# Kernel optimization log

Hardware: AMD Instinct MI355X
Metric: run time of the kernel (lower is better)

The kernel has to match this reference:

```python
import jax, jax.numpy as jnp
import numpy as np


def setup_inputs() -> dict:
    key = jax.random.key(0)
    ks = jax.random.split(key, 6)
    B, S, H, F, E = 4, 2048, 1024, 4096, 8
    x = jax.random.normal(ks[0], (B, S, H), dtype=jnp.float32)
    Wr = jax.random.normal(ks[1], (H, E), dtype=jnp.float32) * (1.0 / np.sqrt(H))
    br = jnp.zeros((E,), dtype=jnp.float32)
    W1 = jax.random.normal(ks[2], (E, H, F), dtype=jnp.float32) * (1.0 / np.sqrt(H))
    b1 = jnp.zeros((E, F), dtype=jnp.float32)
    W2 = jax.random.normal(ks[3], (E, F, H), dtype=jnp.float32) * (1.0 / np.sqrt(F))
    b2 = jnp.zeros((E, H), dtype=jnp.float32)
    b_buf = jnp.zeros((E,), dtype=jnp.float32)  # load-balancing bias buffer, zero-init
    return {"x": x, "b_buf": b_buf, "Wr": Wr, "br": br,
            "W1": W1, "b1": b1, "W2": W2, "b2": b2, "k": 2}


def reference(x, b_buf, Wr, br, W1, b1, W2, b2, k):
    # Router
    scores = jnp.einsum('bsh,he->bse', x, Wr) + br          # [B,S,E]
    probs = jax.nn.softmax(scores, axis=-1)
    # load_balancing: expert selection uses biased scores (b_buf pre-update)
    _, expert_id = jax.lax.top_k(probs + b_buf, k)          # [B,S,k] int
    # combine weights use unbiased probs
    p, _ = jax.lax.top_k(probs, k)                          # [B,S,k]
    # Dense-dispatch reference: run every expert MLP on all tokens,
    # then select via one-hot mask (same math as gather/scatter dispatch).
    h1 = jnp.einsum('bsh,ehf->ebsf', x, W1) + b1[:, None, None, :]
    h1 = jax.nn.gelu(h1, approximate=False)                 # torch nn.GELU = exact
    out_e = jnp.einsum('ebsf,efh->ebsh', h1, W2) + b2[:, None, None, :]
    E = W1.shape[0]
    onehot = (expert_id[None, :, :, :] == jnp.arange(E)[:, None, None, None]).astype(x.dtype)  # [E,B,S,k]
    out_k = jnp.einsum('ebsk,ebsh->bskh', onehot, out_e)    # scatter-combine per slot
    w = p / jnp.sum(p, axis=-1, keepdims=True)              # normalize top-k probs
    return jnp.einsum('bsk,bskh->bsh', w, out_k)
```

## Files before the change

kernel.cpp:

```cpp
#include <hip/hip_runtime.h>
#include <stdint.h>

#define NTOK 8192
#define H_ 1024
#define F_ 4096
#define E_ 8
#define VCAP 18432
#define VMBLK 72
#define MT 144
#define NCOMP 16384

using f32x4  = __attribute__((ext_vector_type(4))) float;
using short8 = __attribute__((ext_vector_type(8))) short;

typedef __attribute__((address_space(1))) const uint32_t gu32;
typedef __attribute__((address_space(3))) uint32_t lu32;

__device__ __forceinline__ void glds16(const void* g, void* l) {
  __builtin_amdgcn_global_load_lds((gu32*)g, (lu32*)l, 16, 0, 0);
}

__device__ __forceinline__ ushort f2bf(float f) {
  union { float f; uint32_t u; } v; v.f = f;
  uint32_t r = (v.u + 0x7FFFu + ((v.u >> 16) & 1u)) >> 16;
  return (ushort)r;
}

__device__ __forceinline__ float gelu_t(float x) {
  float u = 0.7978845608028654f * (x + 0.044715f * x * x * x);
  float e = exp2f(u * 2.885390081777927f);
  float th = 1.0f - 2.0f / (1.0f + e);
  return 0.5f * x * (1.0f + th);
}

__global__ __launch_bounds__(256) void k_prep(const float* __restrict__ W1,
                                              const float* __restrict__ W2,
                                              ushort* __restrict__ W1T,
                                              ushort* __restrict__ W2T,
                                              const float* __restrict__ x,
                                              const float* __restrict__ Wr,
                                              const float* __restrict__ br,
                                              const float* __restrict__ bbuf,
                                              int* cnt, int* te, float* tw,
                                              int* cur, int* tok, float* wl,
                                              int* v2c) {
  int bid = blockIdx.x;
  if (bid < VMBLK) {
    int i = bid * 256 + threadIdx.x;
    if (i < E_) { cnt[i] = 0; cur[i] = 0; }
    if (i < VCAP) { tok[i] = -1; wl[i] = 0.f; v2c[i] = -1; }
  }
  if (bid >= 16384) {
    int wid = threadIdx.x >> 6, lane = threadIdx.x & 63;
    int t = (bid - 16384) * 4 + wid;
    const float* xp = x + (size_t)t * H_;
    double acc[E_];
#pragma unroll
    for (int e = 0; e < E_; e++) acc[e] = 0.0;
    for (int j = lane; j < H_; j += 64) {
      float xv = xp[j];
      const float4 w0 = *(const float4*)&Wr[j * 8];
      const float4 w1 = *(const float4*)&Wr[j * 8 + 4];
      acc[0] += (double)xv * (double)w0.x;
      acc[1] += (double)xv * (double)w0.y;
      acc[2] += (double)xv * (double)w0.z;
      acc[3] += (double)xv * (double)w0.w;
      acc[4] += (double)xv * (double)w1.x;
      acc[5] += (double)xv * (double)w1.y;
      acc[6] += (double)xv * (double)w1.z;
      acc[7] += (double)xv * (double)w1.w;
    }
#pragma unroll
    for (int e = 0; e < E_; e++)
      for (int s = 32; s > 0; s >>= 1) acc[e] += __shfl_xor(acc[e], s);
    if (lane == 0) {
      double s[E_], m = -1e300;
      for (int e = 0; e < E_; e++) { s[e] = acc[e] + (double)br[e]; if (s[e] > m) m = s[e]; }
      double pe[E_], sum = 0.0;
      for (int e = 0; e < E_; e++) { pe[e] = exp(s[e] - m); sum += pe[e]; }
      double pr[E_], bb[E_];
      for (int e = 0; e < E_; e++) { pr[e] = pe[e] / sum; bb[e] = pr[e] + (double)bbuf[e]; }
      int e0 = 0;
      for (int e = 1; e < E_; e++) if (bb[e] > bb[e0]) e0 = e;
      int e1 = (e0 == 0) ? 1 : 0;
      for (int e = 0; e < E_; e++) if (e != e0 && bb[e] > bb[e1]) e1 = e;
      int a0 = 0;
      for (int e = 1; e < E_; e++) if (pr[e] > pr[a0]) a0 = e;
      int a1 = (a0 == 0) ? 1 : 0;
      for (int e = 0; e < E_; e++) if (e != a0 && pr[e] > pr[a1]) a1 = e;
      double iv = 1.0 / (pr[a0] + pr[a1]);
      te[t * 2] = e0; te[t * 2 + 1] = e1;
      tw[t * 2] = (float)(pr[a0] * iv); tw[t * 2 + 1] = (float)(pr[a1] * iv);
      atomicAdd(&cnt[e0], 1); atomicAdd(&cnt[e1], 1);
    }
    return;
  }
  const float* W; ushort* WT; int R, C, nx, t;
  if (bid < 8192) { W = W1; WT = W1T; R = 1024; C = 4096; nx = 64; t = bid; }
  else            { W = W2; WT = W2T; R = 4096; C = 1024; nx = 16; t = bid - 8192; }
  int e = t >> 10, r = t & 1023;
  int c0 = (r % nx) * 64, r0 = (r / nx) * 64;

  __shared__ float tb[64][65];
  const float* Wp = W + (size_t)e * R * C;
  ushort* Tp = WT + (size_t)e * R * C;
  int tx = threadIdx.x & 15, ty = threadIdx.x >> 4;
#pragma unroll
  for (int i = 0; i < 4; i++) {
    int lr = ty + i * 16;
    const float4 v = *(const float4*)&Wp[(size_t)(r0 + lr) * C + c0 + tx * 4];
    tb[lr][tx * 4 + 0] = v.x; tb[lr][tx * 4 + 1] = v.y;
    tb[lr][tx * 4 + 2] = v.z; tb[lr][tx * 4 + 3] = v.w;
  }
  __syncthreads();
#pragma unroll
  for (int i = 0; i < 4; i++) {
    int lc = ty + i * 16;
    ushort4 o;
    o.x = f2bf(tb[tx * 4 + 0][lc]);
    o.y = f2bf(tb[tx * 4 + 1][lc]);
    o.z = f2bf(tb[tx * 4 + 2][lc]);
    o.w = f2bf(tb[tx * 4 + 3][lc]);
    *(ushort4*)&Tp[(size_t)(c0 + lc) * R + r0 + tx * 4] = o;
  }
}

__global__ void k_offsets(const int* cnt, int* off, int* coff) {
  if (threadIdx.x == 0 && blockIdx.x == 0) {
    int o = 0, c = 0;
    for (int e = 0; e < E_; e++) {
      off[e] = o; coff[e] = c;
      o += ((cnt[e] + 255) >> 8) << 8;
      c += cnt[e];
    }
    off[E_] = o; coff[E_] = c;
  }
}

__global__ void k_build(const int* __restrict__ te, const float* __restrict__ tw,
                        const int* __restrict__ off, const int* __restrict__ coff,
                        int* cur, int* tok, float* wl, int* v2c, int* ctok) {
  int t = blockIdx.x * 256 + threadIdx.x;
  if (t >= NTOK) return;
#pragma unroll
  for (int s = 0; s < 2; s++) {
    int e = te[t * 2 + s];
    int slot = atomicAdd(&cur[e], 1);
    int vp = off[e] + slot;
    int cp = coff[e] + slot;
    tok[vp] = t; wl[vp] = tw[t * 2 + s]; v2c[vp] = cp; ctok[cp] = t;
  }
}

__global__ __launch_bounds__(256) void k_gather(const float* __restrict__ x,
                                                const int* __restrict__ ctok,
                                                ushort* __restrict__ Xg,
                                                float* __restrict__ out) {
  int gid = blockIdx.x * 256 + threadIdx.x;
  if (gid < NTOK * H_ / 4) {
    float4 z; z.x = 0.f; z.y = 0.f; z.z = 0.f; z.w = 0.f;
    ((float4*)out)[gid] = z;
  }
  int row = blockIdx.x;
  int t = ctok[row];
  const float4* src = (const float4*)(x + (size_t)t * H_);
  ushort4* dst = (ushort4*)(Xg + (size_t)row * H_);
  int i = threadIdx.x;
  float4 v = src[i];
  ushort4 o; o.x = f2bf(v.x); o.y = f2bf(v.y); o.z = f2bf(v.z); o.w = f2bf(v.w);
  dst[i] = o;
}

template <int MODE>
__global__ __launch_bounds__(256, 3) void k_gemm(const ushort* __restrict__ A,
                                                 const ushort* __restrict__ BT,
                                                 const float* __restrict__ bias,
                                                 ushort* __restrict__ h1,
                                                 float* __restrict__ Out,
                                                 const int* __restrict__ off,
                                                 const int* __restrict__ v2c,
                                                 const int* __restrict__ tok,
                                                 const float* __restrict__ wl,
                                                 int K, int N, int NTe) {
  __shared__ __align__(16) ushort As[128 * 64];
  __shared__ __align__(16) ushort Bs[128 * 64];

  int nwg = gridDim.x;
  int cpx = nwg >> 3;
  int bid = blockIdx.x;
  int lid = (bid & 7) * cpx + (bid >> 3);
  int ng = lid / (MT * 8), r = lid % (MT * 8);
  int m = r >> 3;
  int ne = (ng << 3) + (r & 7);
  int row0 = m << 7;
  if (row0 >= off[E_]) return;
  int e = 0;
  while (off[e + 1] <= row0) e++;
  int n0, k0, nk;
  if (MODE == 0) { n0 = ne << 7; k0 = 0; nk = K >> 6; }
  else           { n0 = (ne & 7) << 7; k0 = (ne >> 3) * (K >> 1); nk = K >> 7; }
  const ushort* Bp = BT + (size_t)e * (size_t)N * (size_t)K;

  int tid = threadIdx.x, lane = tid & 63, w = tid >> 6;
  int wr = w >> 1, wc = w & 1;

  f32x4 acc[4][4];
#pragma unroll
  for (int mm = 0; mm < 4; mm++)
#pragma unroll
    for (int nn = 0; nn < 4; nn++) acc[mm][nn] = (f32x4){0.f, 0.f, 0.f, 0.f};

  int urow = (w << 3) + (lane >> 3);
  int sc = (lane & 7) ^ (urow & 7);
  const char *aP0, *aP1, *aP2, *aP3, *bP0, *bP1, *bP2, *bP3;
  {
    size_t kb = (size_t)k0 * 2 + (size_t)sc * 16;
    int c0 = v2c[row0 + 0 * 32 + urow];  if (c0 < 0) c0 = 0;
    int c1 = v2c[row0 + 1 * 32 + urow];  if (c1 < 0) c1 = 0;
    int c2 = v2c[row0 + 2 * 32 + urow];  if (c2 < 0) c2 = 0;
    int c3 = v2c[row0 + 3 * 32 + urow];  if (c3 < 0) c3 = 0;
    aP0 = (const char*)(A + (size_t)c0 * K) + kb;
    aP1 = (const char*)(A + (size_t)c1 * K) + kb;
    aP2 = (const char*)(A + (size_t)c2 * K) + kb;
    aP3 = (const char*)(A + (size_t)c3 * K) + kb;
    bP0 = (const char*)(Bp + (size_t)(n0 + 0 * 32 + urow) * K) + kb;
    bP1 = (const char*)(Bp + (size_t)(n0 + 1 * 32 + urow) * K) + kb;
    bP2 = (const char*)(Bp + (size_t)(n0 + 2 * 32 + urow) * K) + kb;
    bP3 = (const char*)(Bp + (size_t)(n0 + 3 * 32 + urow) * K) + kb;
  }

  int fr = lane & 15, fq = lane >> 4;
  int frs = fr & 7;

  for (int kk = 0; kk < nk; ++kk) {
    size_t kbo = (size_t)kk * 128;
    if (kk) __syncthreads();
    glds16(aP0 + kbo, (char*)As + 0 * 4096 + (w << 10));
    glds16(bP0 + kbo, (char*)Bs + 0 * 4096 + (w << 10));
    glds16(aP1 + kbo, (char*)As + 1 * 4096 + (w << 10));
    glds16(bP1 + kbo, (char*)Bs + 1 * 4096 + (w << 10));
    glds16(aP2 + kbo, (char*)As + 2 * 4096 + (w << 10));
    glds16(bP2 + kbo, (char*)Bs + 2 * 4096 + (w << 10));
    glds16(aP3 + kbo, (char*)As + 3 * 4096 + (w << 10));
    glds16(bP3 + kbo, (char*)Bs + 3 * 4096 + (w << 10));
    __syncthreads();
#pragma unroll
    for (int ks = 0; ks < 2; ++ks) {
      short8 af[4], bf[4];
      int kc = (((ks << 2) + fq) ^ frs) << 3;
#pragma unroll
      for (int i = 0; i < 4; ++i)
        af[i] = *(const short8*)&As[((wr << 6) + i * 16 + fr) * 64 + kc];
#pragma unroll
      for (int i = 0; i < 4; ++i)
        bf[i] = *(const short8*)&Bs[((wc << 6) + i * 16 + fr) * 64 + kc];
#pragma unroll
      for (int mm = 0; mm < 4; ++mm)
#pragma unroll
        for (int nn = 0; nn < 4; ++nn)
          acc[mm][nn] = __builtin_amdgcn_mfma_f32_16x16x32_bf16(af[mm], bf[nn], acc[mm][nn], 0, 0, 0);
    }
  }

  const float* bp = bias + (size_t)e * N;
  int cb = n0 + (wc << 6);
  if (MODE == 0) {
#pragma unroll
    for (int mm = 0; mm < 4; mm++) {
#pragma unroll
      for (int j = 0; j < 4; j++) {
        int vr = row0 + (wr << 6) + mm * 16 + (fq << 2) + j;
        int cr = v2c[vr];
        if (cr < 0) continue;
        ushort* hp = h1 + (size_t)cr * N + cb;
#pragma unroll
        for (int nn = 0; nn < 4; nn++) {
          float v = acc[mm][nn][j] + bp[cb + nn * 16 + fr];
          hp[nn * 16 + fr] = f2bf(gelu_t(v));
        }
      }
    }
  } else {
    bool addb = (k0 == 0);
#pragma unroll
    for (int mm = 0; mm < 4; mm++) {
#pragma unroll
      for (int j = 0; j < 4; j++) {
        int vr = row0 + (wr << 6) + mm * 16 + (fq << 2) + j;
        int t2 = tok[vr];
        if (t2 < 0) continue;
        float wgt = wl[vr];
#pragma unroll
        for (int nn = 0; nn < 4; nn++) {
          int c = cb + nn * 16 + fr;
          float v = acc[mm][nn][j] + (addb ? bp[c] : 0.f);
          atomicAdd(&Out[(size_t)t2 * (size_t)N + c], wgt * v);
        }
      }
    }
  }
}

extern "C" void kernel_launch(void* const* d_in, const int* in_sizes, int n_in,
                              void* d_out, int out_size, void* d_ws, size_t ws_size,
                              hipStream_t stream) {
  (void)in_sizes; (void)n_in; (void)out_size; (void)ws_size;
  const float* x    = (const float*)d_in[0];
  const float* bbuf = (const float*)d_in[1];
  const float* Wr   = (const float*)d_in[2];
  const float* br   = (const float*)d_in[3];
  const float* W1   = (const float*)d_in[4];
  const float* b1   = (const float*)d_in[5];
  const float* W2   = (const float*)d_in[6];
  const float* b2   = (const float*)d_in[7];
  float* out = (float*)d_out;

  char* ws = (char*)d_ws;
  ushort* W1T = (ushort*)ws;
  ushort* W2T = (ushort*)(ws + 67108864);
  ushort* Xg  = (ushort*)(ws + 134217728);
  ushort* h1  = (ushort*)(ws + 167772160);
  char* meta  = ws + 301989888;
  int*   cnt  = (int*)(meta);
  int*   off  = (int*)(meta + 64);
  int*   coff = (int*)(meta + 128);
  int*   cur  = (int*)(meta + 192);
  int*   te   = (int*)(meta + 256);
  float* tw   = (float*)(meta + 65792);
  int*   tok  = (int*)(meta + 131328);
  float* wl   = (float*)(meta + 205056);
  int*   v2c  = (int*)(meta + 278784);
  int*   ctok = (int*)(meta + 352512);

  k_prep<<<18432, 256, 0, stream>>>(W1, W2, W1T, W2T, x, Wr, br, bbuf,
                                    cnt, te, tw, cur, tok, wl, v2c);
  k_offsets<<<1, 64, 0, stream>>>(cnt, off, coff);
  k_build<<<NTOK / 256, 256, 0, stream>>>(te, tw, off, coff, cur, tok, wl, v2c, ctok);
  k_gather<<<NCOMP, 256, 0, stream>>>(x, ctok, Xg, out);
  k_gemm<0><<<32 * MT, 256, 0, stream>>>(Xg, W1T, b1, h1, nullptr,
                                         off, v2c, nullptr, nullptr,
                                         H_, F_, 32);
  k_gemm<1><<<16 * MT, 256, 0, stream>>>(h1, W2T, b2, nullptr, out,
                                         off, v2c, tok, wl,
                                         F_, H_, 16);
}
```

Measured before the change: 872.3 us.

## Overlap W2 transpose-convert with first expert GEMM via interleaved blocks

Moves the W2 fp32-to-bf16 transpose out of the prep kernel and interleaves those tiles with the first GEMM's workgroups, 16 transpose blocks per 9 GEMM blocks. The bandwidth-bound conversion can then run alongside the compute-bound GEMM1 instead of serially before it. Metadata initialisation is replaced by hipMemsetAsync calls. In exchange, GEMM1's grid grows and its block scheduling mixes in memory-heavy tiles, and the extra memset launches add overhead.

```diff
diff --git a/kernel.cpp b/kernel.cpp
--- a/kernel.cpp
+++ b/kernel.cpp
@@ -9,6 +9,7 @@
 #define VMBLK 72
 #define MT 144
 #define NCOMP 16384
+#define NWG1 4608
 
 using f32x4  = __attribute__((ext_vector_type(4))) float;
 using short8 = __attribute__((ext_vector_type(8))) short;
@@ -33,26 +34,47 @@
   return 0.5f * x * (1.0f + th);
 }
 
-__global__ __launch_bounds__(256) void k_prep(const float* __restrict__ W1,
-                                              const float* __restrict__ W2,
-                                              ushort* __restrict__ W1T,
-                                              ushort* __restrict__ W2T,
-                                              const float* __restrict__ x,
-                                              const float* __restrict__ Wr,
-                                              const float* __restrict__ br,
-                                              const float* __restrict__ bbuf,
-                                              int* cnt, int* te, float* tw,
-                                              int* cur, int* tok, float* wl,
-                                              int* v2c) {
+__device__ __forceinline__ void transcvt_tile(const float* __restrict__ W,
+                                              ushort* __restrict__ WT,
+                                              int R, int C, int nx, int t,
+                                              float (*tb)[65]) {
+  int e = t >> 10, r = t & 1023;
+  int c0 = (r % nx) * 64, r0 = (r / nx) * 64;
+  const float* Wp = W + (size_t)e * R * C;
+  ushort* Tp = WT + (size_t)e * R * C;
+  int tx = threadIdx.x & 15, ty = threadIdx.x >> 4;
+#pragma unroll
+  for (int i = 0; i < 4; i++) {
+    int lr = ty + i * 16;
+    const float4 v = *(const float4*)&Wp[(size_t)(r0 + lr) * C + c0 + tx * 4];
+    tb[lr][tx * 4 + 0] = v.x; tb[lr][tx * 4 + 1] = v.y;
+    tb[lr][tx * 4 + 2] = v.z; tb[lr][tx * 4 + 3] = v.w;
+  }
+  __syncthreads();
+#pragma unroll
+  for (int i = 0; i < 4; i++) {
+    int lc = ty + i * 16;
+    ushort4 o;
+    o.x = f2bf(tb[tx * 4 + 0][lc]);
+    o.y = f2bf(tb[tx * 4 + 1][lc]);
+    o.z = f2bf(tb[tx * 4 + 2][lc]);
+    o.w = f2bf(tb[tx * 4 + 3][lc]);
+    *(ushort4*)&Tp[(size_t)(c0 + lc) * R + r0 + tx * 4] = o;
+  }
+}
+
+__global__ __launch_bounds__(256) void k_prep2(const float* __restrict__ W1,
+                                               ushort* __restrict__ W1T,
+                                               const float* __restrict__ x,
+                                               const float* __restrict__ Wr,
+                                               const float* __restrict__ br,
+                                               const float* __restrict__ bbuf,
+                                               int* cnt, int* te, float* tw) {
+  __shared__ float tb[64][65];
   int bid = blockIdx.x;
-  if (bid < VMBLK) {
-    int i = bid * 256 + threadIdx.x;
-    if (i < E_) { cnt[i] = 0; cur[i] = 0; }
-    if (i < VCAP) { tok[i] = -1; wl[i] = 0.f; v2c[i] = -1; }
-  }
-  if (bid >= 16384) {
+  if (bid < 2048) {
     int wid = threadIdx.x >> 6, lane = threadIdx.x & 63;
-    int t = (bid - 16384) * 4 + wid;
+    int t = bid * 4 + wid;
     const float* xp = x + (size_t)t * H_;
     double acc[E_];
 #pragma unroll
@@ -95,34 +117,7 @@
     }
     return;
   }
-  const float* W; ushort* WT; int R, C, nx, t;
-  if (bid < 8192) { W = W1; WT = W1T; R = 1024; C = 4096; nx = 64; t = bid; }
-  else            { W = W2; WT = W2T; R = 4096; C = 1024; nx = 16; t = bid - 8192; }
-  int e = t >> 10, r = t & 1023;
-  int c0 = (r % nx) * 64, r0 = (r / nx) * 64;
-
-  __shared__ float tb[64][65];
-  const float* Wp = W + (size_t)e * R * C;
-  ushort* Tp = WT + (size_t)e * R * C;
-  int tx = threadIdx.x & 15, ty = threadIdx.x >> 4;
-#pragma unroll
-  for (int i = 0; i < 4; i++) {
-    int lr = ty + i * 16;
-    const float4 v = *(const float4*)&Wp[(size_t)(r0 + lr) * C + c0 + tx * 4];
-    tb[lr][tx * 4 + 0] = v.x; tb[lr][tx * 4 + 1] = v.y;
-    tb[lr][tx * 4 + 2] = v.z; tb[lr][tx * 4 + 3] = v.w;
-  }
-  __syncthreads();
-#pragma unroll
-  for (int i = 0; i < 4; i++) {
-    int lc = ty + i * 16;
-    ushort4 o;
-    o.x = f2bf(tb[tx * 4 + 0][lc]);
-    o.y = f2bf(tb[tx * 4 + 1][lc]);
-    o.z = f2bf(tb[tx * 4 + 2][lc]);
-    o.w = f2bf(tb[tx * 4 + 3][lc]);
-    *(ushort4*)&Tp[(size_t)(c0 + lc) * R + r0 + tx * 4] = o;
-  }
+  transcvt_tile(W1, W1T, 1024, 4096, 64, bid - 2048, tb);
 }
 
 __global__ void k_offsets(const int* cnt, int* off, int* coff) {
@@ -171,20 +166,128 @@
   dst[i] = o;
 }
 
-template <int MODE>
-__global__ __launch_bounds__(256, 3) void k_gemm(const ushort* __restrict__ A,
-                                                 const ushort* __restrict__ BT,
-                                                 const float* __restrict__ bias,
-                                                 ushort* __restrict__ h1,
-                                                 float* __restrict__ Out,
-                                                 const int* __restrict__ off,
-                                                 const int* __restrict__ v2c,
-                                                 const int* __restrict__ tok,
-                                                 const float* __restrict__ wl,
-                                                 int K, int N, int NTe) {
+__global__ __launch_bounds__(256, 3) void k_gemm1f(const ushort* __restrict__ A,
+                                                   const ushort* __restrict__ BT,
+                                                   const float* __restrict__ bias,
+                                                   ushort* __restrict__ h1,
+                                                   const int* __restrict__ off,
+                                                   const int* __restrict__ v2c,
+                                                   const float* __restrict__ W2,
+                                                   ushort* __restrict__ W2T) {
+  __shared__ __align__(16) char smem[32768];
+  int g = blockIdx.x / 25, idx = blockIdx.x % 25;
+  if (idx >= 9) {
+    float (*tb)[65] = (float(*)[65])smem;
+    transcvt_tile(W2, W2T, 4096, 1024, 16, g * 16 + (idx - 9), tb);
+    return;
+  }
+  const int K = H_, N = F_;
+  ushort* As = (ushort*)smem;
+  ushort* Bs = (ushort*)(smem + 16384);
+  int gid = g * 9 + idx;
+  int cpx = NWG1 >> 3;
+  int lid = (gid & 7) * cpx + (gid >> 3);
+  int ng = lid / (MT * 8), r = lid % (MT * 8);
+  int m = r >> 3;
+  int ne = (ng << 3) + (r & 7);
+  int row0 = m << 7;
+  if (row0 >= off[E_]) return;
+  int e = 0;
+  while (off[e + 1] <= row0) e++;
+  int n0 = ne << 7, nk = K >> 6;
+  const ushort* Bp = BT + (size_t)e * (size_t)N * (size_t)K;
+
+  int lane = threadIdx.x & 63, w = threadIdx.x >> 6;
+  int wr = w >> 1, wc = w & 1;
+
+  f32x4 acc[4][4];
+#pragma unroll
+  for (int mm = 0; mm < 4; mm++)
+#pragma unroll
+    for (int nn = 0; nn < 4; nn++) acc[mm][nn] = (f32x4){0.f, 0.f, 0.f, 0.f};
+
+  int urow = (w << 3) + (lane >> 3);
+  int sc = (lane & 7) ^ (urow & 7);
+  const char *aP0, *aP1, *aP2, *aP3, *bP0, *bP1, *bP2, *bP3;
+  {
+    size_t kb = (size_t)sc * 16;
+    int c0 = v2c[row0 + 0 * 32 + urow];  if (c0 < 0) c0 = 0;
+    int c1 = v2c[row0 + 1 * 32 + urow];  if (c1 < 0) c1 = 0;
+    int c2 = v2c[row0 + 2 * 32 + urow];  if (c2 < 0) c2 = 0;
+    int c3 = v2c[row0 + 3 * 32 + urow];  if (c3 < 0) c3 = 0;
+    aP0 = (const char*)(A + (size_t)c0 * K) + kb;
+    aP1 = (const char*)(A + (size_t)c1 * K) + kb;
+    aP2 = (const char*)(A + (size_t)c2 * K) + kb;
+    aP3 = (const char*)(A + (size_t)c3 * K) + kb;
+    bP0 = (const char*)(Bp + (size_t)(n0 + 0 * 32 + urow) * K) + kb;
+    bP1 = (const char*)(Bp + (size_t)(n0 + 1 * 32 + urow) * K) + kb;
+    bP2 = (const char*)(Bp + (size_t)(n0 + 2 * 32 + urow) * K) + kb;
+    bP3 = (const char*)(Bp + (size_t)(n0 + 3 * 32 + urow) * K) + kb;
+  }
+
+  int fr = lane & 15, fq = lane >> 4;
+  int frs = fr & 7;
+
+  for (int kk = 0; kk < nk; ++kk) {
+    size_t kbo = (size_t)kk * 128;
+    if (kk) __syncthreads();
+    glds16(aP0 + kbo, (char*)As + 0 * 4096 + (w << 10));
+    glds16(bP0 + kbo, (char*)Bs + 0 * 4096 + (w << 10));
+    glds16(aP1 + kbo, (char*)As + 1 * 4096 + (w << 10));
+    glds16(bP1 + kbo, (char*)Bs + 1 * 4096 + (w << 10));
+    glds16(aP2 + kbo, (char*)As + 2 * 4096 + (w << 10));
+    glds16(bP2 + kbo, (char*)Bs + 2 * 4096 + (w << 10));
+    glds16(aP3 + kbo, (char*)As + 3 * 4096 + (w << 10));
+    glds16(bP3 + kbo, (char*)Bs + 3 * 4096 + (w << 10));
+    __syncthreads();
+#pragma unroll
+    for (int ks = 0; ks < 2; ++ks) {
+      short8 af[4], bf[4];
+      int kc = (((ks << 2) + fq) ^ frs) << 3;
+#pragma unroll
+      for (int i = 0; i < 4; ++i)
+        af[i] = *(const short8*)&As[((wr << 6) + i * 16 + fr) * 64 + kc];
+#pragma unroll
+      for (int i = 0; i < 4; ++i)
+        bf[i] = *(const short8*)&Bs[((wc << 6) + i * 16 + fr) * 64 + kc];
+#pragma unroll
+      for (int mm = 0; mm < 4; ++mm)
+#pragma unroll
+        for (int nn = 0; nn < 4; ++nn)
+          acc[mm][nn] = __builtin_amdgcn_mfma_f32_16x16x32_bf16(af[mm], bf[nn], acc[mm][nn], 0, 0, 0);
+    }
+  }
+
+  const float* bp = bias + (size_t)e * N;
+  int cb = n0 + (wc << 6);
+#pragma unroll
+  for (int mm = 0; mm < 4; mm++) {
+#pragma unroll
+    for (int j = 0; j < 4; j++) {
+      int vr = row0 + (wr << 6) + mm * 16 + (fq << 2) + j;
+      int cr = v2c[vr];
+      if (cr < 0) continue;
+      ushort* hp = h1 + (size_t)cr * N + cb;
+#pragma unroll
+      for (int nn = 0; nn < 4; nn++) {
+        float v = acc[mm][nn][j] + bp[cb + nn * 16 + fr];
+        hp[nn * 16 + fr] = f2bf(gelu_t(v));
+      }
+    }
+  }
+}
+
+__global__ __launch_bounds__(256, 3) void k_gemm2(const ushort* __restrict__ A,
+                                                  const ushort* __restrict__ BT,
+                                                  const float* __restrict__ bias,
+                                                  float* __restrict__ Out,
+                                                  const int* __restrict__ off,
+                                                  const int* __restrict__ v2c,
+                                                  const int* __restrict__ tok,
+                                                  const float* __restrict__ wl) {
   __shared__ __align__(16) ushort As[128 * 64];
   __shared__ __align__(16) ushort Bs[128 * 64];
-
+  const int K = F_, N = H_, NTe = 16;
   int nwg = gridDim.x;
   int cpx = nwg >> 3;
   int bid = blockIdx.x;
@@ -192,16 +295,15 @@
   int ng = lid / (MT * 8), r = lid % (MT * 8);
   int m = r >> 3;
   int ne = (ng << 3) + (r & 7);
+  (void)NTe;
   int row0 = m << 7;
   if (row0 >= off[E_]) return;
   int e = 0;
   while (off[e + 1] <= row0) e++;
-  int n0, k0, nk;
-  if (MODE == 0) { n0 = ne << 7; k0 = 0; nk = K >> 6; }
-  else           { n0 = (ne & 7) << 7; k0 = (ne >> 3) * (K >> 1); nk = K >> 7; }
+  int n0 = (ne & 7) << 7, k0 = (ne >> 3) * (K >> 1), nk = K >> 7;
   const ushort* Bp = BT + (size_t)e * (size_t)N * (size_t)K;
 
-  int tid = threadIdx.x, lane = tid & 63, w = tid >> 6;
+  int lane = threadIdx.x & 63, w = threadIdx.x >> 6;
   int wr = w >> 1, wc = w & 1;
 
   f32x4 acc[4][4];
@@ -264,38 +366,20 @@
 
   const float* bp = bias + (size_t)e * N;
   int cb = n0 + (wc << 6);
-  if (MODE == 0) {
-#pragma unroll
-    for (int mm = 0; mm < 4; mm++) {
-#pragma unroll
-      for (int j = 0; j < 4; j++) {
-        int vr = row0 + (wr << 6) + mm * 16 + (fq << 2) + j;
-        int cr = v2c[vr];
-        if (cr < 0) continue;
-        ushort* hp = h1 + (size_t)cr * N + cb;
-#pragma unroll
-        for (int nn = 0; nn < 4; nn++) {
-          float v = acc[mm][nn][j] + bp[cb + nn * 16 + fr];
-          hp[nn * 16 + fr] = f2bf(gelu_t(v));
-        }
-      }
-    }
-  } else {
-    bool addb = (k0 == 0);
-#pragma unroll
-    for (int mm = 0; mm < 4; mm++) {
-#pragma unroll
-      for (int j = 0; j < 4; j++) {
-        int vr = row0 + (wr << 6) + mm * 16 + (fq << 2) + j;
-        int t2 = tok[vr];
-        if (t2 < 0) continue;
-        float wgt = wl[vr];
-#pragma unroll
-        for (int nn = 0; nn < 4; nn++) {
-          int c = cb + nn * 16 + fr;
-          float v = acc[mm][nn][j] + (addb ? bp[c] : 0.f);
-          atomicAdd(&Out[(size_t)t2 * (size_t)N + c], wgt * v);
-        }
+  bool addb = (k0 == 0);
+#pragma unroll
+  for (int mm = 0; mm < 4; mm++) {
+#pragma unroll
+    for (int j = 0; j < 4; j++) {
+      int vr = row0 + (wr << 6) + mm * 16 + (fq << 2) + j;
+      int t2 = tok[vr];
+      if (t2 < 0) continue;
+      float wgt = wl[vr];
+#pragma unroll
+      for (int nn = 0; nn < 4; nn++) {
+        int c = cb + nn * 16 + fr;
+        float v = acc[mm][nn][j] + (addb ? bp[c] : 0.f);
+        atomicAdd(&Out[(size_t)t2 * (size_t)N + c], wgt * v);
       }
     }
   }
@@ -332,15 +416,15 @@
   int*   v2c  = (int*)(meta + 278784);
   int*   ctok = (int*)(meta + 352512);
 
-  k_prep<<<18432, 256, 0, stream>>>(W1, W2, W1T, W2T, x, Wr, br, bbuf,
-                                    cnt, te, tw, cur, tok, wl, v2c);
+  hipMemsetAsync(meta, 0, 256, stream);
+  hipMemsetAsync(tok, 0xFF, VCAP * 4, stream);
+  hipMemsetAsync(wl, 0, VCAP * 4, stream);
+  hipMemsetAsync(v2c, 0xFF, VCAP * 4, stream);
+
+  k_prep2<<<10240, 256, 0, stream>>>(W1, W1T, x, Wr, br, bbuf, cnt, te, tw);
   k_offsets<<<1, 64, 0, stream>>>(cnt, off, coff);
   k_build<<<NTOK / 256, 256, 0, stream>>>(te, tw, off, coff, cur, tok, wl, v2c, ctok);
   k_gather<<<NCOMP, 256, 0, stream>>>(x, ctok, Xg, out);
-  k_gemm<0><<<32 * MT, 256, 0, stream>>>(Xg, W1T, b1, h1, nullptr,
-                                         off, v2c, nullptr, nullptr,
-                                         H_, F_, 32);
-  k_gemm<1><<<16 * MT, 256, 0, stream>>>(h1, W2T, b2, nullptr, out,
-                                         off, v2c, tok, wl,
-                                         F_, H_, 16);
-}
+  k_gemm1f<<<12800, 256, 0, stream>>>(Xg, W1T, b1, h1, off, v2c, W2, W2T);
+  k_gemm2<<<16 * MT, 256, 0, stream>>>(h1, W2T, b2, out, off, v2c, tok, wl);
+}
```

Result: no change. 885.5 us (+1.5%).
